# Optimization experiments

Measured on AMD Instinct MI355X. Metric: run time of the kernel, lower is better.

Reference implementation:

```python
import math
import jax, jax.numpy as jnp
import numpy as np

B, L, D_MODEL, H = 8, 4096, 1024, 16
D_HEAD = D_MODEL // H
FACTOR = 5
U = max(int(math.ceil(math.log(L))) * FACTOR, 1)  # 45 = sample_k = n_top


def setup_inputs() -> dict:
    key = jax.random.key(0)
    ks = jax.random.split(key, 12)
    s = 0.02
    return {
        "Q": jax.random.normal(ks[0], (B, L, D_MODEL), jnp.float32),
        "K": jax.random.normal(ks[1], (B, L, D_MODEL), jnp.float32),
        "V": jax.random.normal(ks[2], (B, L, D_MODEL), jnp.float32),
        "Wq": jax.random.normal(ks[3], (D_MODEL, D_MODEL), jnp.float32) * s,
        "bq": jnp.zeros((D_MODEL,), jnp.float32),
        "Wk": jax.random.normal(ks[4], (D_MODEL, D_MODEL), jnp.float32) * s,
        "bk": jnp.zeros((D_MODEL,), jnp.float32),
        "Wv": jax.random.normal(ks[5], (D_MODEL, D_MODEL), jnp.float32) * s,
        "bv": jnp.zeros((D_MODEL,), jnp.float32),
        "Wo": jax.random.normal(ks[6], (D_MODEL, D_MODEL), jnp.float32) * s,
        "bo": jnp.zeros((D_MODEL,), jnp.float32),
        "index_sample": jax.random.randint(ks[7], (U,), 0, L, dtype=jnp.int32),
    }


def reference(Q, K, V, Wq, bq, Wk, bk, Wv, bv, Wo, bo, index_sample):
    scale = 1.0 / math.sqrt(D_HEAD)
    # projections (torch Linear: x @ W.T + b), split into heads -> [B,H,L,D]
    q = (Q @ Wq.T + bq).reshape(B, L, H, D_HEAD).transpose(0, 2, 1, 3)
    k = (K @ Wk.T + bk).reshape(B, L, H, D_HEAD).transpose(0, 2, 1, 3)
    v = (V @ Wv.T + bv).reshape(B, L, H, D_HEAD).transpose(0, 2, 1, 3)
    # _prob_QK: sample U keys, score every query against them
    k_samp = k[:, :, index_sample, :]                        # [B,H,U,D]
    qk_samp = jnp.einsum('bhqd,bhsd->bhqs', q, k_samp)       # [B,H,L,U]
    M = qk_samp.max(-1) - qk_samp.mean(-1)                   # [B,H,L] max-mean sparsity metric
    _, m_top = jax.lax.top_k(M, U)                           # [B,H,U] top query indices
    # gather top queries, reduced attention over ALL keys
    q_red = jnp.take_along_axis(q, m_top[..., None], axis=2)  # [B,H,U,D]
    scores = jnp.einsum('bhud,bhkd->bhuk', q_red, k) * scale  # [B,H,U,L]
    attn = jax.nn.softmax(scores, axis=-1)
    ctx = jnp.einsum('bhuk,bhkd->bhud', attn, v)              # [B,H,U,D]
    ctx_mean = ctx.mean(axis=2)                               # [B,H,D]
    ctx_flat = ctx_mean.transpose(0, 2, 1).reshape(B, D_MODEL)  # transpose(1,2).view(B,-1)
    return ctx_flat @ Wo.T + bo                               # [B, d_model]
```

## Files before the change

kernel.cpp:

```cpp
#include <hip/hip_runtime.h>
#include <stdint.h>

#define B_ 8
#define L_ 4096
#define DM_ 1024
#define H_ 16
#define DH_ 64
#define U_ 45
#define BH_ 128
#define GROWS_ 384
#define GM_ 3072
#define CHUNKS_ 2

typedef unsigned short u16;
typedef unsigned int u32;
typedef __attribute__((ext_vector_type(8))) short short8;
typedef __attribute__((ext_vector_type(4))) float f32x4;
typedef __attribute__((ext_vector_type(8))) float f32x8;

__device__ __forceinline__ u16 f2bf_rne(float x){
  u32 u = __float_as_uint(x);
  return (u16)((u + 0x7FFFu + ((u >> 16) & 1u)) >> 16);
}
__device__ __forceinline__ float bf2f(u16 v){ return __uint_as_float(((u32)v) << 16); }

__device__ __forceinline__ void gload_lds16(const void* g, void* l){
  auto gp = (const __attribute__((address_space(1))) u32*)(uintptr_t)g;
  auto lp = (__attribute__((address_space(3))) u32*)(u32)(uintptr_t)l;
  __builtin_amdgcn_global_load_lds(gp, lp, 16, 0, 0);
}

__device__ __forceinline__ void split1(float x, u16& h, u16& l){
  h = f2bf_rne(x);
  l = f2bf_rne(x - bf2f(h));
}

__global__ void prep_w(const float* __restrict__ Wq, const float* __restrict__ Wk,
                       const float* __restrict__ Wv,
                       u16* __restrict__ WQH, u16* __restrict__ WQL,
                       u16* __restrict__ WKH, u16* __restrict__ WKL,
                       u16* __restrict__ WVH){
  const int i = (blockIdx.x * 256 + threadIdx.x) * 4;
  float4 a; ushort4 h, l;
  a = *(const float4*)(Wq + i);
  split1(a.x, h.x, l.x); split1(a.y, h.y, l.y); split1(a.z, h.z, l.z); split1(a.w, h.w, l.w);
  *(ushort4*)(WQH + i) = h; *(ushort4*)(WQL + i) = l;
  a = *(const float4*)(Wk + i);
  split1(a.x, h.x, l.x); split1(a.y, h.y, l.y); split1(a.z, h.z, l.z); split1(a.w, h.w, l.w);
  *(ushort4*)(WKH + i) = h; *(ushort4*)(WKL + i) = l;
  a = *(const float4*)(Wv + i);
  split1(a.x, h.x, l.x); split1(a.y, h.y, l.y); split1(a.z, h.z, l.z); split1(a.w, h.w, l.w);
  *(ushort4*)(WVH + i) = h;
}

__global__ void gather_rows(const float* __restrict__ K, const int* __restrict__ IDX,
                            float* __restrict__ GATH){
  const int blk = blockIdx.x;
  const int b = blk / U_, u = blk % U_;
  const int t = threadIdx.x;
  const int row = IDX[u];
  const float4* src = (const float4*)(K + ((size_t)b * L_ + row) * DM_);
  float4* dst = (float4*)(GATH + ((size_t)(b * GROWS_ + u)) * DM_);
  dst[t] = src[t];
}

template<int PASSES, int OUTMODE>
__launch_bounds__(256, 2)
__global__ void gemm_proj(const float* __restrict__ A, const u16* __restrict__ BHp,
                          const u16* __restrict__ BLp, const float* __restrict__ bias,
                          void* __restrict__ outp){
  const int n0 = blockIdx.x * 128;
  const int m0 = blockIdx.y * 128;
  const int t = threadIdx.x;
  const int w = t >> 6, lane = t & 63;
  const int wr = w >> 1, wc = w & 1;

  __shared__ __attribute__((aligned(16))) float As[128 * 64];
  __shared__ __attribute__((aligned(16))) u16   Bhs[128 * 64];
  __shared__ __attribute__((aligned(16))) u16   Bls[(PASSES == 3) ? (128 * 64) : 64];

  f32x4 acc[4][4];
#pragma unroll
  for (int i = 0; i < 4; i++)
#pragma unroll
    for (int j = 0; j < 4; j++) acc[i][j] = (f32x4){0.f, 0.f, 0.f, 0.f};

  const int arow = lane >> 4;
  const int acol = (lane & 15) * 4;
  const int brow = lane >> 3;
  const int bcol = (lane & 7) * 8;

  for (int kt = 0; kt < 16; kt++){
    const int k0 = kt * 64;
#pragma unroll
    for (int ii = 0; ii < 8; ii++){
      const int nn = w * 8 + ii;
      const float* gp = A + (size_t)(m0 + 4 * nn + arow) * DM_ + (k0 + acol);
      gload_lds16(gp, As + nn * 256);
    }
#pragma unroll
    for (int ii = 0; ii < 4; ii++){
      const int nn = w * 4 + ii;
      const size_t go = (size_t)(n0 + 8 * nn + brow) * DM_ + (k0 + bcol);
      gload_lds16(BHp + go, Bhs + nn * 512);
      if constexpr (PASSES == 3) gload_lds16(BLp + go, Bls + nn * 512);
    }
    __syncthreads();

#pragma unroll
    for (int ks = 0; ks < 2; ks++){
      const int kk = ks * 32 + (lane >> 4) * 8;
      short8 ah[4], al[4];
#pragma unroll
      for (int i = 0; i < 4; i++){
        const float* ap = As + (wr * 64 + i * 16 + (lane & 15)) * 64 + kk;
        f32x8 x = *(const f32x8*)ap;
        short8 h, l;
#pragma unroll
        for (int c = 0; c < 8; c++){
          const u32 ub = __float_as_uint(x[c]);
          h[c] = (short)(ub >> 16);
          if constexpr (PASSES == 3){
            const float r = x[c] - __uint_as_float(ub & 0xFFFF0000u);
            l[c] = (short)(__float_as_uint(r) >> 16);
          }
        }
        ah[i] = h;
        if constexpr (PASSES == 3) al[i] = l;
      }
      short8 bh8[4], bl8[4];
#pragma unroll
      for (int j = 0; j < 4; j++){
        const int bo = (wc * 64 + j * 16 + (lane & 15)) * 64 + kk;
        bh8[j] = *(const short8*)(Bhs + bo);
        if constexpr (PASSES == 3) bl8[j] = *(const short8*)(Bls + bo);
      }
#pragma unroll
      for (int i = 0; i < 4; i++)
#pragma unroll
        for (int j = 0; j < 4; j++){
          acc[i][j] = __builtin_amdgcn_mfma_f32_16x16x32_bf16(ah[i], bh8[j], acc[i][j], 0, 0, 0);
          if constexpr (PASSES == 3){
            acc[i][j] = __builtin_amdgcn_mfma_f32_16x16x32_bf16(ah[i], bl8[j], acc[i][j], 0, 0, 0);
            acc[i][j] = __builtin_amdgcn_mfma_f32_16x16x32_bf16(al[i], bh8[j], acc[i][j], 0, 0, 0);
          }
        }
    }
    __syncthreads();
  }

  if constexpr (OUTMODE == 3){
    u16* tb = (u16*)As;
    const int b = m0 >> 12;
    const int l0 = m0 & 4095;
#pragma unroll
    for (int p = 0; p < 2; p++){
      if (wc == p){
#pragma unroll
        for (int j = 0; j < 4; j++){
          const int cl = j * 16 + (lane & 15);
          const float bv = bias[n0 + p * 64 + cl];
#pragma unroll
          for (int i = 0; i < 4; i++){
#pragma unroll
            for (int r = 0; r < 4; r++){
              const int gl = wr * 64 + i * 16 + (lane >> 4) * 4 + r;
              tb[cl * 136 + gl] = f2bf_rne(acc[i][j][r] + bv);
            }
          }
        }
      }
      __syncthreads();
      {
        const int cl = t >> 2;
        const int c = n0 + p * 64 + cl;
        const int h = c >> 6, d = c & 63;
        u16* dst = (u16*)outp + ((size_t)((b * H_ + h) * DH_ + d)) * L_ + l0;
#pragma unroll
        for (int k = 0; k < 4; k++){
          const int ch = (t & 3) + k * 4;
          *(short8*)(dst + ch * 8) = *(const short8*)(tb + cl * 136 + ch * 8);
        }
      }
      __syncthreads();
    }
  } else {
#pragma unroll
    for (int j = 0; j < 4; j++){
      const int c = n0 + wc * 64 + j * 16 + (lane & 15);
      const float bv = bias[c];
#pragma unroll
      for (int i = 0; i < 4; i++){
        const int mb = m0 + wr * 64 + i * 16 + (lane >> 4) * 4;
#pragma unroll
        for (int r = 0; r < 4; r++){
          const int g = mb + r;
          const float val = acc[i][j][r] + bv;
          if constexpr (OUTMODE == 2){
            ((float*)outp)[(size_t)g * DM_ + c] = val;
          } else {
            const int b = g >> 12, l2 = g & 4095;
            const int h = c >> 6, d = c & 63;
            const size_t oi = (((size_t)(b * H_ + h)) * L_ + l2) * DH_ + d;
            if constexpr (OUTMODE == 0) ((float*)outp)[oi] = val;
            else ((u16*)outp)[oi] = (u16)(__float_as_uint(val) >> 16);
          }
        }
      }
    }
  }
}

__global__ void compute_m(const float* __restrict__ QF, const float* __restrict__ KSAMP,
                          float* __restrict__ MBUF){
  const int bx = blockIdx.x;
  const int bh = bx >> 4, lp = bx & 15;
  const int b = bh >> 4, h = bh & 15;
  const int t = threadIdx.x;
  __shared__ float ks[U_ * DH_];
  for (int i = t; i < U_ * DH_; i += 256){
    const int u = i >> 6, d = i & 63;
    ks[i] = KSAMP[((size_t)(b * GROWS_ + u)) * DM_ + h * DH_ + d];
  }
  __syncthreads();
  const int l = lp * 256 + t;
  const float* q = QF + ((size_t)bh * L_ + l) * DH_;
  float4 qv[16];
#pragma unroll
  for (int c = 0; c < 16; c++) qv[c] = *(const float4*)(q + c * 4);
  float mx = -1e30f, sm = 0.f;
  for (int u = 0; u < U_; u++){
    const float* kp = ks + u * 64;
    float acc = 0.f;
#pragma unroll
    for (int c = 0; c < 16; c++){
      const float4 kv = *(const float4*)(kp + c * 4);
      acc += qv[c].x * kv.x + qv[c].y * kv.y + qv[c].z * kv.z + qv[c].w * kv.w;
    }
    mx = fmaxf(mx, acc); sm += acc;
  }
  MBUF[(size_t)bh * L_ + l] = mx - sm * (1.0f / 45.0f);
}

__global__ void topk45(const float* __restrict__ MBUF, int* __restrict__ MTOP){
  const int bh = blockIdx.x;
  const int t = threadIdx.x;
  __shared__ float Mv[L_];
  __shared__ float rv[256];
  __shared__ int ri[256];
  for (int i = t; i < L_; i += 256) Mv[i] = MBUF[(size_t)bh * L_ + i];
  __syncthreads();
  for (int it = 0; it < U_; it++){
    float bv = -1e30f; int bi = 0;
#pragma unroll
    for (int c = 0; c < 16; c++){
      const int idx = t * 16 + c;
      const float v = Mv[idx];
      if (v > bv){ bv = v; bi = idx; }
    }
    rv[t] = bv; ri[t] = bi;
    __syncthreads();
    for (int off = 128; off > 0; off >>= 1){
      if (t < off){
        const float v2 = rv[t + off]; const int i2 = ri[t + off];
        if (v2 > rv[t] || (v2 == rv[t] && i2 < ri[t])){ rv[t] = v2; ri[t] = i2; }
      }
      __syncthreads();
    }
    if (t == 0){ MTOP[bh * U_ + it] = ri[0]; Mv[ri[0]] = -1e30f; }
    __syncthreads();
  }
}

__launch_bounds__(256, 2)
__global__ void attn_fused(const float* __restrict__ QF, const u16* __restrict__ KB,
                           const u16* __restrict__ VT, const int* __restrict__ MTOP,
                           float* __restrict__ MLP, float* __restrict__ CTXP){
  const int bh = blockIdx.x;
  const int chunk = blockIdx.y;
  const int t = threadIdx.x, w = t >> 6, lane = t & 63;
  const int m16 = lane & 15, q4 = lane >> 4;

  __shared__ __attribute__((aligned(16))) float qs[48 * 68];
  __shared__ __attribute__((aligned(16))) u16 ps[4][48 * 72];

  for (int i = t; i < 48 * 64; i += 256){
    const int r = i >> 6, d = i & 63;
    float v = 0.f;
    if (r < U_) v = QF[((size_t)bh * L_ + MTOP[bh * U_ + r]) * DH_ + d] * 0.125f;
    qs[r * 68 + d] = v;
  }
  __syncthreads();

  short8 qh[3][2], ql[3][2];
#pragma unroll
  for (int i = 0; i < 3; i++)
#pragma unroll
    for (int ks = 0; ks < 2; ks++){
      const float* ap = qs + (i * 16 + m16) * 68 + ks * 32 + q4 * 8;
      f32x8 x = *(const f32x8*)ap;
      short8 h, l;
#pragma unroll
      for (int c = 0; c < 8; c++){
        const u32 ub = __float_as_uint(x[c]);
        h[c] = (short)(ub >> 16);
        const float r = x[c] - __uint_as_float(ub & 0xFFFF0000u);
        l[c] = (short)(__float_as_uint(r) >> 16);
      }
      qh[i][ks] = h; ql[i][ks] = l;
    }

  float m_run[3][4], l_run[3][4];
  f32x4 O[3][4];
#pragma unroll
  for (int i = 0; i < 3; i++)
#pragma unroll
    for (int r = 0; r < 4; r++){
      m_run[i][r] = -1e30f; l_run[i][r] = 0.f;
      O[i][r] = (f32x4){0.f, 0.f, 0.f, 0.f};
    }

  const u16* kb = KB + (size_t)bh * L_ * DH_;
  const u16* vt = VT + (size_t)bh * DH_ * L_;
  const int TPW = L_ / (CHUNKS_ * 4 * 64);
  u16* pw = ps[w];

  for (int tt = 0; tt < TPW; tt++){
    const int t0 = ((chunk * 4 + w) * TPW + tt) * 64;
    f32x4 S[3][4];
#pragma unroll
    for (int i = 0; i < 3; i++)
#pragma unroll
      for (int jt = 0; jt < 4; jt++) S[i][jt] = (f32x4){0.f, 0.f, 0.f, 0.f};
#pragma unroll
    for (int ks = 0; ks < 2; ks++){
      short8 kf[4];
#pragma unroll
      for (int jt = 0; jt < 4; jt++)
        kf[jt] = *(const short8*)(kb + (size_t)(t0 + jt * 16 + m16) * DH_ + ks * 32 + q4 * 8);
#pragma unroll
      for (int i = 0; i < 3; i++)
#pragma unroll
        for (int jt = 0; jt < 4; jt++){
          S[i][jt] = __builtin_amdgcn_mfma_f32_16x16x32_bf16(qh[i][ks], kf[jt], S[i][jt], 0, 0, 0);
          S[i][jt] = __builtin_amdgcn_mfma_f32_16x16x32_bf16(ql[i][ks], kf[jt], S[i][jt], 0, 0, 0);
        }
    }
#pragma unroll
    for (int i = 0; i < 3; i++){
      float mnew[4], alpha[4], psum[4];
#pragma unroll
      for (int r = 0; r < 4; r++){
        float mx = fmaxf(fmaxf(S[i][0][r], S[i][1][r]), fmaxf(S[i][2][r], S[i][3][r]));
        mx = fmaxf(mx, __shfl_xor(mx, 1));
        mx = fmaxf(mx, __shfl_xor(mx, 2));
        mx = fmaxf(mx, __shfl_xor(mx, 4));
        mx = fmaxf(mx, __shfl_xor(mx, 8));
        mnew[r] = fmaxf(m_run[i][r], mx);
        alpha[r] = __expf(m_run[i][r] - mnew[r]);
        m_run[i][r] = mnew[r];
        l_run[i][r] *= alpha[r];
        psum[r] = 0.f;
      }
#pragma unroll
      for (int jo = 0; jo < 4; jo++)
#pragma unroll
        for (int r = 0; r < 4; r++) O[i][jo][r] *= alpha[r];
#pragma unroll
      for (int jt = 0; jt < 4; jt++)
#pragma unroll
        for (int r = 0; r < 4; r++){
          const float pv = __expf(S[i][jt][r] - mnew[r]);
          const u16 pq = f2bf_rne(pv);
          psum[r] += bf2f(pq);
          pw[(i * 16 + q4 * 4 + r) * 72 + jt * 16 + m16] = pq;
        }
#pragma unroll
      for (int r = 0; r < 4; r++){
        float s = psum[r];
        s += __shfl_xor(s, 1); s += __shfl_xor(s, 2);
        s += __shfl_xor(s, 4); s += __shfl_xor(s, 8);
        l_run[i][r] += s;
      }
    }
#pragma unroll
    for (int ks = 0; ks < 2; ks++){
      short8 pa[3], vf[4];
#pragma unroll
      for (int i = 0; i < 3; i++)
        pa[i] = *(const short8*)(pw + (i * 16 + m16) * 72 + ks * 32 + q4 * 8);
#pragma unroll
      for (int jo = 0; jo < 4; jo++)
        vf[jo] = *(const short8*)(vt + (size_t)(jo * 16 + m16) * L_ + t0 + ks * 32 + q4 * 8);
#pragma unroll
      for (int i = 0; i < 3; i++)
#pragma unroll
        for (int jo = 0; jo < 4; jo++)
          O[i][jo] = __builtin_amdgcn_mfma_f32_16x16x32_bf16(pa[i], vf[jo], O[i][jo], 0, 0, 0);
    }
  }

  const int state = (bh * CHUNKS_ + chunk) * 4 + w;
  float* mlp = MLP + (size_t)state * 48 * 2;
  float* ctxp = CTXP + (size_t)state * 48 * 64;
#pragma unroll
  for (int i = 0; i < 3; i++)
#pragma unroll
    for (int r = 0; r < 4; r++){
      const int row = i * 16 + q4 * 4 + r;
      if (m16 == 0){ mlp[row * 2] = m_run[i][r]; mlp[row * 2 + 1] = l_run[i][r]; }
#pragma unroll
      for (int jo = 0; jo < 4; jo++)
        ctxp[row * 64 + jo * 16 + m16] = O[i][jo][r];
    }
}

__global__ void attn_combine(const float* __restrict__ MLP, const float* __restrict__ CTXP,
                             float* __restrict__ CTXF){
  const int bh = blockIdx.x;
  const int b = bh >> 4, h = bh & 15;
  const int t = threadIdx.x;
  const int col = t & 63, rg = t >> 6;
  const int NS = CHUNKS_ * 4;
  __shared__ float ml[8 * 48 * 2];
  __shared__ float red[4][64];
  for (int i = t; i < NS * 48 * 2; i += 256) ml[i] = MLP[(size_t)bh * NS * 48 * 2 + i];
  __syncthreads();
  float acc = 0.f;
  for (int rr = 0; rr < 12; rr++){
    const int row = rg * 12 + rr;
    if (row >= U_) break;
    float M = -1e30f;
#pragma unroll
    for (int s = 0; s < NS; s++) M = fmaxf(M, ml[s * 96 + row * 2]);
    float num = 0.f, den = 0.f;
#pragma unroll
    for (int s = 0; s < NS; s++){
      const float wgt = __expf(ml[s * 96 + row * 2] - M);
      num += wgt * CTXP[((size_t)bh * NS + s) * 48 * 64 + row * 64 + col];
      den += wgt * ml[s * 96 + row * 2 + 1];
    }
    acc += num / den;
  }
  red[rg][col] = acc;
  __syncthreads();
  if (t < 64){
    const float v = (red[0][t] + red[1][t] + red[2][t] + red[3][t]) * (1.0f / 45.0f);
    CTXF[b * DM_ + t * H_ + h] = v;
  }
}

__global__ void s4_out(const float* __restrict__ CTXF, const float* __restrict__ Wo,
                       const float* __restrict__ bo, float* __restrict__ out){
  const int jb = blockIdx.x;
  const int b = blockIdx.y;
  const int t = threadIdx.x;
  __shared__ float cx[DM_];
  for (int i = t; i < DM_; i += 256) cx[i] = CTXF[b * DM_ + i];
  __syncthreads();
  const int j = jb * 256 + t;
  const float* wrow = Wo + (size_t)j * DM_;
  float acc = bo[j];
  for (int c = 0; c < 256; c++){
    const float4 wv = *(const float4*)(wrow + c * 4);
    const float4 cv = *(const float4*)(cx + c * 4);
    acc += wv.x * cv.x + wv.y * cv.y + wv.z * cv.z + wv.w * cv.w;
  }
  out[b * DM_ + j] = acc;
}

extern "C" void kernel_launch(void* const* d_in, const int* in_sizes, int n_in,
                              void* d_out, int out_size, void* d_ws, size_t ws_size,
                              hipStream_t stream){
  const float* Q  = (const float*)d_in[0];
  const float* K  = (const float*)d_in[1];
  const float* V  = (const float*)d_in[2];
  const float* Wq = (const float*)d_in[3];
  const float* bq = (const float*)d_in[4];
  const float* Wk = (const float*)d_in[5];
  const float* bk = (const float*)d_in[6];
  const float* Wv = (const float*)d_in[7];
  const float* bv = (const float*)d_in[8];
  const float* Wo = (const float*)d_in[9];
  const float* bo = (const float*)d_in[10];
  const int* IDX  = (const int*)d_in[11];
  float* out = (float*)d_out;

  char* p = (char*)d_ws;
  auto alloc = [&](size_t bytes) -> char* {
    char* r = p; p += (bytes + 255) & ~(size_t)255; return r;
  };
  u16*  WQH  = (u16*)alloc((size_t)DM_ * DM_ * 2);
  u16*  WQL  = (u16*)alloc((size_t)DM_ * DM_ * 2);
  u16*  WKH  = (u16*)alloc((size_t)DM_ * DM_ * 2);
  u16*  WKL  = (u16*)alloc((size_t)DM_ * DM_ * 2);
  u16*  WVH  = (u16*)alloc((size_t)DM_ * DM_ * 2);
  float* QF  = (float*)alloc((size_t)BH_ * L_ * DH_ * 4);
  u16*  KB   = (u16*)alloc((size_t)BH_ * L_ * DH_ * 2);
  u16*  VT   = (u16*)alloc((size_t)BH_ * DH_ * L_ * 2);
  float* GATH = (float*)alloc((size_t)GM_ * DM_ * 4);
  float* KSAMP= (float*)alloc((size_t)GM_ * DM_ * 4);
  float* MBUF = (float*)alloc((size_t)BH_ * L_ * 4);
  int*   MTOP = (int*)alloc((size_t)BH_ * U_ * 4);
  float* MLP  = (float*)alloc((size_t)BH_ * CHUNKS_ * 4 * 48 * 2 * 4);
  float* CTXP = (float*)alloc((size_t)BH_ * CHUNKS_ * 4 * 48 * 64 * 4);
  float* CTXF = (float*)alloc((size_t)B_ * DM_ * 4);

  prep_w<<<dim3(1024), dim3(256), 0, stream>>>(Wq, Wk, Wv, WQH, WQL, WKH, WKL, WVH);
  gather_rows<<<dim3(B_ * U_), dim3(256), 0, stream>>>(K, IDX, GATH);
  gemm_proj<3, 0><<<dim3(8, 256), dim3(256), 0, stream>>>(Q, WQH, WQL, bq, (void*)QF);
  gemm_proj<1, 1><<<dim3(8, 256), dim3(256), 0, stream>>>(K, WKH, (const u16*)nullptr, bk, (void*)KB);
  gemm_proj<1, 3><<<dim3(8, 256), dim3(256), 0, stream>>>(V, WVH, (const u16*)nullptr, bv, (void*)VT);
  gemm_proj<3, 2><<<dim3(8, GM_ / 128), dim3(256), 0, stream>>>(GATH, WKH, WKL, bk, (void*)KSAMP);
  compute_m<<<dim3(BH_ * 16), dim3(256), 0, stream>>>(QF, KSAMP, MBUF);
  topk45<<<dim3(BH_), dim3(256), 0, stream>>>(MBUF, MTOP);
  attn_fused<<<dim3(BH_, CHUNKS_), dim3(256), 0, stream>>>(QF, KB, VT, MTOP, MLP, CTXP);
  attn_combine<<<dim3(BH_), dim3(256), 0, stream>>>(MLP, CTXP, CTXF);
  s4_out<<<dim3(4, 8), dim3(256), 0, stream>>>(CTXF, Wo, bo, out);
}
```

Baseline: 1.187 ms.

## Fuse max-mean sparsity metric into Q projection epilogue and swizzle GEMM LDS

The sampled-key score computation (compute_m) moves into the Q projection GEMM epilogue. Each block stages its projected Q tile in LDS and scores it against pre-split bf16 hi/lo sampled keys with MFMA, writing the max-mean metric directly. This drops the separate kernel and its re-read of QF. The sampled-key GEMM now runs on a padded 48-row gather (3 row blocks instead of 24), and a new ksprep kernel splits it into hi/lo bf16. GEMM LDS tiles get XOR swizzling to avoid bank conflicts, and topk uses wave shuffles instead of an LDS tree reduction. The cost is a larger LDS footprint for the Q GEMM (68KB), which could lower occupancy.

```diff
diff --git a/kernel.cpp b/kernel.cpp
--- a/kernel.cpp
+++ b/kernel.cpp
@@ -8,15 +8,12 @@
 #define DH_ 64
 #define U_ 45
 #define BH_ 128
-#define GROWS_ 384
-#define GM_ 3072
 #define CHUNKS_ 2
 
 typedef unsigned short u16;
 typedef unsigned int u32;
 typedef __attribute__((ext_vector_type(8))) short short8;
 typedef __attribute__((ext_vector_type(4))) float f32x4;
-typedef __attribute__((ext_vector_type(8))) float f32x8;
 
 __device__ __forceinline__ u16 f2bf_rne(float x){
   u32 u = __float_as_uint(x);
@@ -56,28 +53,35 @@
 __global__ void gather_rows(const float* __restrict__ K, const int* __restrict__ IDX,
                             float* __restrict__ GATH){
   const int blk = blockIdx.x;
-  const int b = blk / U_, u = blk % U_;
+  const int b = blk / 48, u = blk % 48;
   const int t = threadIdx.x;
-  const int row = IDX[u];
-  const float4* src = (const float4*)(K + ((size_t)b * L_ + row) * DM_);
-  float4* dst = (float4*)(GATH + ((size_t)(b * GROWS_ + u)) * DM_);
-  dst[t] = src[t];
-}
-
-template<int PASSES, int OUTMODE>
+  float4 v = make_float4(0.f, 0.f, 0.f, 0.f);
+  if (u < U_){
+    const int row = IDX[u];
+    v = ((const float4*)(K + ((size_t)b * L_ + row) * DM_))[t];
+  }
+  ((float4*)(GATH + ((size_t)(b * 48 + u)) * DM_))[t] = v;
+}
+
+template<int PASSES, int OUTMODE, bool WITHM>
 __launch_bounds__(256, 2)
 __global__ void gemm_proj(const float* __restrict__ A, const u16* __restrict__ BHp,
                           const u16* __restrict__ BLp, const float* __restrict__ bias,
-                          void* __restrict__ outp){
+                          void* __restrict__ outp,
+                          const u16* __restrict__ KSH, const u16* __restrict__ KSL,
+                          float* __restrict__ MBUF){
+  constexpr int LDSB = WITHM ? 69632 : (PASSES == 3 ? 65536 : 49152);
+  __shared__ __attribute__((aligned(16))) char smem[LDSB];
+  float* As = (float*)smem;
+  u16* Bhs = (u16*)(smem + 32768);
+  u16* Bls = (u16*)(smem + 49152);
+
   const int n0 = blockIdx.x * 128;
   const int m0 = blockIdx.y * 128;
   const int t = threadIdx.x;
   const int w = t >> 6, lane = t & 63;
   const int wr = w >> 1, wc = w & 1;
-
-  __shared__ __attribute__((aligned(16))) float As[128 * 64];
-  __shared__ __attribute__((aligned(16))) u16   Bhs[128 * 64];
-  __shared__ __attribute__((aligned(16))) u16   Bls[(PASSES == 3) ? (128 * 64) : 64];
+  const int m16 = lane & 15, q4 = lane >> 4;
 
   f32x4 acc[4][4];
 #pragma unroll
@@ -86,22 +90,26 @@
     for (int j = 0; j < 4; j++) acc[i][j] = (f32x4){0.f, 0.f, 0.f, 0.f};
 
   const int arow = lane >> 4;
-  const int acol = (lane & 15) * 4;
+  const int acN  = lane & 15;
   const int brow = lane >> 3;
-  const int bcol = (lane & 7) * 8;
+  const int bcN  = lane & 7;
 
   for (int kt = 0; kt < 16; kt++){
     const int k0 = kt * 64;
 #pragma unroll
     for (int ii = 0; ii < 8; ii++){
       const int nn = w * 8 + ii;
-      const float* gp = A + (size_t)(m0 + 4 * nn + arow) * DM_ + (k0 + acol);
+      const int rl = 4 * nn + arow;
+      const int c2 = acN ^ (rl & 15);
+      const float* gp = A + (size_t)(m0 + rl) * DM_ + (k0 + c2 * 4);
       gload_lds16(gp, As + nn * 256);
     }
 #pragma unroll
     for (int ii = 0; ii < 4; ii++){
       const int nn = w * 4 + ii;
-      const size_t go = (size_t)(n0 + 8 * nn + brow) * DM_ + (k0 + bcol);
+      const int rb = 8 * nn + brow;
+      const int cb = bcN ^ (brow & 7);
+      const size_t go = (size_t)(n0 + rb) * DM_ + (k0 + cb * 8);
       gload_lds16(BHp + go, Bhs + nn * 512);
       if constexpr (PASSES == 3) gload_lds16(BLp + go, Bls + nn * 512);
     }
@@ -109,31 +117,35 @@
 
 #pragma unroll
     for (int ks = 0; ks < 2; ks++){
-      const int kk = ks * 32 + (lane >> 4) * 8;
+      const int gc0 = ks * 8 + q4 * 2;
       short8 ah[4], al[4];
 #pragma unroll
       for (int i = 0; i < 4; i++){
-        const float* ap = As + (wr * 64 + i * 16 + (lane & 15)) * 64 + kk;
-        f32x8 x = *(const f32x8*)ap;
+        const float* base = As + (wr * 64 + i * 16 + m16) * 64;
+        const f32x4 xlo = *(const f32x4*)(base + (gc0 ^ m16) * 4);
+        const f32x4 xhi = *(const f32x4*)(base + ((gc0 + 1) ^ m16) * 4);
+        float xx[8] = {xlo[0], xlo[1], xlo[2], xlo[3], xhi[0], xhi[1], xhi[2], xhi[3]};
         short8 h, l;
 #pragma unroll
         for (int c = 0; c < 8; c++){
-          const u32 ub = __float_as_uint(x[c]);
+          const u32 ub = __float_as_uint(xx[c]);
           h[c] = (short)(ub >> 16);
           if constexpr (PASSES == 3){
-            const float r = x[c] - __uint_as_float(ub & 0xFFFF0000u);
+            const float r = xx[c] - __uint_as_float(ub & 0xFFFF0000u);
             l[c] = (short)(__float_as_uint(r) >> 16);
           }
         }
         ah[i] = h;
         if constexpr (PASSES == 3) al[i] = l;
       }
+      const int gcb = ks * 4 + q4;
       short8 bh8[4], bl8[4];
 #pragma unroll
       for (int j = 0; j < 4; j++){
-        const int bo = (wc * 64 + j * 16 + (lane & 15)) * 64 + kk;
-        bh8[j] = *(const short8*)(Bhs + bo);
-        if constexpr (PASSES == 3) bl8[j] = *(const short8*)(Bls + bo);
+        const int rowb = wc * 64 + j * 16 + m16;
+        const int pos = gcb ^ (m16 & 7);
+        bh8[j] = *(const short8*)(Bhs + rowb * 64 + pos * 8);
+        if constexpr (PASSES == 3) bl8[j] = *(const short8*)(Bls + rowb * 64 + pos * 8);
       }
 #pragma unroll
       for (int i = 0; i < 4; i++)
@@ -149,8 +161,9 @@
     __syncthreads();
   }
 
+  float* mt = (float*)smem + w * (64 * 68);
   if constexpr (OUTMODE == 3){
-    u16* tb = (u16*)As;
+    u16* tb = (u16*)smem;
     const int b = m0 >> 12;
     const int l0 = m0 & 4095;
 #pragma unroll
@@ -158,13 +171,13 @@
       if (wc == p){
 #pragma unroll
         for (int j = 0; j < 4; j++){
-          const int cl = j * 16 + (lane & 15);
+          const int cl = j * 16 + m16;
           const float bv = bias[n0 + p * 64 + cl];
 #pragma unroll
           for (int i = 0; i < 4; i++){
 #pragma unroll
             for (int r = 0; r < 4; r++){
-              const int gl = wr * 64 + i * 16 + (lane >> 4) * 4 + r;
+              const int gl = wr * 64 + i * 16 + q4 * 4 + r;
               tb[cl * 136 + gl] = f2bf_rne(acc[i][j][r] + bv);
             }
           }
@@ -187,11 +200,11 @@
   } else {
 #pragma unroll
     for (int j = 0; j < 4; j++){
-      const int c = n0 + wc * 64 + j * 16 + (lane & 15);
+      const int c = n0 + wc * 64 + j * 16 + m16;
       const float bv = bias[c];
 #pragma unroll
       for (int i = 0; i < 4; i++){
-        const int mb = m0 + wr * 64 + i * 16 + (lane >> 4) * 4;
+        const int mb = m0 + wr * 64 + i * 16 + q4 * 4;
 #pragma unroll
         for (int r = 0; r < 4; r++){
           const int g = mb + r;
@@ -205,69 +218,123 @@
             if constexpr (OUTMODE == 0) ((float*)outp)[oi] = val;
             else ((u16*)outp)[oi] = (u16)(__float_as_uint(val) >> 16);
           }
-        }
-      }
-    }
-  }
-}
-
-__global__ void compute_m(const float* __restrict__ QF, const float* __restrict__ KSAMP,
-                          float* __restrict__ MBUF){
-  const int bx = blockIdx.x;
-  const int bh = bx >> 4, lp = bx & 15;
+          if constexpr (WITHM)
+            mt[(i * 16 + q4 * 4 + r) * 68 + (j * 16 + m16)] = val;
+        }
+      }
+    }
+  }
+
+  if constexpr (WITHM){
+    const int bb = m0 >> 12;
+    const int head = (n0 >> 6) + wc;
+    const int bh2 = bb * H_ + head;
+    f32x4 S[4][3];
+#pragma unroll
+    for (int im = 0; im < 4; im++)
+#pragma unroll
+      for (int jt = 0; jt < 3; jt++) S[im][jt] = (f32x4){0.f, 0.f, 0.f, 0.f};
+#pragma unroll
+    for (int ks = 0; ks < 2; ks++){
+      short8 kh3[3], kl3[3];
+#pragma unroll
+      for (int jt = 0; jt < 3; jt++){
+        const size_t ko = ((size_t)bh2 * 48 + jt * 16 + m16) * 64 + ks * 32 + q4 * 8;
+        kh3[jt] = *(const short8*)(KSH + ko);
+        kl3[jt] = *(const short8*)(KSL + ko);
+      }
+#pragma unroll
+      for (int im = 0; im < 4; im++){
+        const float* ap = mt + (im * 16 + m16) * 68 + ks * 32 + q4 * 8;
+        const f32x4 xlo = *(const f32x4*)ap;
+        const f32x4 xhi = *(const f32x4*)(ap + 4);
+        float xx[8] = {xlo[0], xlo[1], xlo[2], xlo[3], xhi[0], xhi[1], xhi[2], xhi[3]};
+        short8 qh, ql;
+#pragma unroll
+        for (int c = 0; c < 8; c++){
+          const u32 ub = __float_as_uint(xx[c]);
+          qh[c] = (short)(ub >> 16);
+          const float r = xx[c] - __uint_as_float(ub & 0xFFFF0000u);
+          ql[c] = (short)(__float_as_uint(r) >> 16);
+        }
+#pragma unroll
+        for (int jt = 0; jt < 3; jt++){
+          S[im][jt] = __builtin_amdgcn_mfma_f32_16x16x32_bf16(qh, kh3[jt], S[im][jt], 0, 0, 0);
+          S[im][jt] = __builtin_amdgcn_mfma_f32_16x16x32_bf16(qh, kl3[jt], S[im][jt], 0, 0, 0);
+          S[im][jt] = __builtin_amdgcn_mfma_f32_16x16x32_bf16(ql, kh3[jt], S[im][jt], 0, 0, 0);
+        }
+      }
+    }
+#pragma unroll
+    for (int im = 0; im < 4; im++)
+#pragma unroll
+      for (int r = 0; r < 4; r++){
+        float mx = -1e30f, sm = 0.f;
+#pragma unroll
+        for (int jt = 0; jt < 3; jt++){
+          const bool ok = (jt < 2) || (m16 < 13);
+          const float v = S[im][jt][r];
+          if (ok){ mx = fmaxf(mx, v); sm += v; }
+        }
+#pragma unroll
+        for (int off = 1; off < 16; off <<= 1){
+          mx = fmaxf(mx, __shfl_xor(mx, off));
+          sm += __shfl_xor(sm, off);
+        }
+        if (m16 == 0){
+          const int l2 = (m0 & 4095) + wr * 64 + im * 16 + q4 * 4 + r;
+          MBUF[(size_t)bh2 * L_ + l2] = mx - sm * (1.0f / 45.0f);
+        }
+      }
+  }
+}
+
+__global__ void ksprep(const float* __restrict__ KSAMP, u16* __restrict__ KSH,
+                       u16* __restrict__ KSL){
+  const int bh = blockIdx.x;
   const int b = bh >> 4, h = bh & 15;
   const int t = threadIdx.x;
-  __shared__ float ks[U_ * DH_];
-  for (int i = t; i < U_ * DH_; i += 256){
+  for (int i = t; i < 48 * 64; i += 256){
     const int u = i >> 6, d = i & 63;
-    ks[i] = KSAMP[((size_t)(b * GROWS_ + u)) * DM_ + h * DH_ + d];
-  }
-  __syncthreads();
-  const int l = lp * 256 + t;
-  const float* q = QF + ((size_t)bh * L_ + l) * DH_;
-  float4 qv[16];
-#pragma unroll
-  for (int c = 0; c < 16; c++) qv[c] = *(const float4*)(q + c * 4);
-  float mx = -1e30f, sm = 0.f;
-  for (int u = 0; u < U_; u++){
-    const float* kp = ks + u * 64;
-    float acc = 0.f;
-#pragma unroll
-    for (int c = 0; c < 16; c++){
-      const float4 kv = *(const float4*)(kp + c * 4);
-      acc += qv[c].x * kv.x + qv[c].y * kv.y + qv[c].z * kv.z + qv[c].w * kv.w;
-    }
-    mx = fmaxf(mx, acc); sm += acc;
-  }
-  MBUF[(size_t)bh * L_ + l] = mx - sm * (1.0f / 45.0f);
+    const float v = (u < U_) ? KSAMP[(size_t)(b * 48 + u) * DM_ + h * DH_ + d] : 0.f;
+    u16 hh, ll; split1(v, hh, ll);
+    KSH[(size_t)bh * 48 * 64 + i] = hh;
+    KSL[(size_t)bh * 48 * 64 + i] = ll;
+  }
 }
 
 __global__ void topk45(const float* __restrict__ MBUF, int* __restrict__ MTOP){
   const int bh = blockIdx.x;
-  const int t = threadIdx.x;
+  const int t = threadIdx.x, w = t >> 6, lane = t & 63;
   __shared__ float Mv[L_];
-  __shared__ float rv[256];
-  __shared__ int ri[256];
+  __shared__ float rv[4];
+  __shared__ int ri[4];
   for (int i = t; i < L_; i += 256) Mv[i] = MBUF[(size_t)bh * L_ + i];
   __syncthreads();
   for (int it = 0; it < U_; it++){
     float bv = -1e30f; int bi = 0;
 #pragma unroll
     for (int c = 0; c < 16; c++){
-      const int idx = t * 16 + c;
+      const int idx = c * 256 + t;
       const float v = Mv[idx];
-      if (v > bv){ bv = v; bi = idx; }
-    }
-    rv[t] = bv; ri[t] = bi;
+      if (v > bv || (v == bv && idx < bi)){ bv = v; bi = idx; }
+    }
+#pragma unroll
+    for (int off = 1; off < 64; off <<= 1){
+      const float ov = __shfl_xor(bv, off);
+      const int oi = __shfl_xor(bi, off);
+      if (ov > bv || (ov == bv && oi < bi)){ bv = ov; bi = oi; }
+    }
+    if (lane == 0){ rv[w] = bv; ri[w] = bi; }
     __syncthreads();
-    for (int off = 128; off > 0; off >>= 1){
-      if (t < off){
-        const float v2 = rv[t + off]; const int i2 = ri[t + off];
-        if (v2 > rv[t] || (v2 == rv[t] && i2 < ri[t])){ rv[t] = v2; ri[t] = i2; }
-      }
-      __syncthreads();
-    }
-    if (t == 0){ MTOP[bh * U_ + it] = ri[0]; Mv[ri[0]] = -1e30f; }
+    if (t == 0){
+      float fb = rv[0]; int fi = ri[0];
+#pragma unroll
+      for (int s = 1; s < 4; s++)
+        if (rv[s] > fb || (rv[s] == fb && ri[s] < fi)){ fb = rv[s]; fi = ri[s]; }
+      MTOP[bh * U_ + it] = fi;
+      Mv[fi] = -1e30f;
+    }
     __syncthreads();
   }
 }
@@ -298,13 +365,15 @@
 #pragma unroll
     for (int ks = 0; ks < 2; ks++){
       const float* ap = qs + (i * 16 + m16) * 68 + ks * 32 + q4 * 8;
-      f32x8 x = *(const f32x8*)ap;
+      const f32x4 xlo = *(const f32x4*)ap;
+      const f32x4 xhi = *(const f32x4*)(ap + 4);
+      float xx[8] = {xlo[0], xlo[1], xlo[2], xlo[3], xhi[0], xhi[1], xhi[2], xhi[3]};
       short8 h, l;
 #pragma unroll
       for (int c = 0; c < 8; c++){
-        const u32 ub = __float_as_uint(x[c]);
+        const u32 ub = __float_as_uint(xx[c]);
         h[c] = (short)(ub >> 16);
-        const float r = x[c] - __uint_as_float(ub & 0xFFFF0000u);
+        const float r = xx[c] - __uint_as_float(ub & 0xFFFF0000u);
         l[c] = (short)(__float_as_uint(r) >> 16);
       }
       qh[i][ks] = h; ql[i][ks] = l;
@@ -498,8 +567,10 @@
   float* QF  = (float*)alloc((size_t)BH_ * L_ * DH_ * 4);
   u16*  KB   = (u16*)alloc((size_t)BH_ * L_ * DH_ * 2);
   u16*  VT   = (u16*)alloc((size_t)BH_ * DH_ * L_ * 2);
-  float* GATH = (float*)alloc((size_t)GM_ * DM_ * 4);
-  float* KSAMP= (float*)alloc((size_t)GM_ * DM_ * 4);
+  float* GATH = (float*)alloc((size_t)B_ * 48 * DM_ * 4);
+  float* KSAMP= (float*)alloc((size_t)B_ * 48 * DM_ * 4);
+  u16*  KSH  = (u16*)alloc((size_t)BH_ * 48 * DH_ * 2);
+  u16*  KSL  = (u16*)alloc((size_t)BH_ * 48 * DH_ * 2);
   float* MBUF = (float*)alloc((size_t)BH_ * L_ * 4);
   int*   MTOP = (int*)alloc((size_t)BH_ * U_ * 4);
   float* MLP  = (float*)alloc((size_t)BH_ * CHUNKS_ * 4 * 48 * 2 * 4);
@@ -507,12 +578,16 @@
   float* CTXF = (float*)alloc((size_t)B_ * DM_ * 4);
 
   prep_w<<<dim3(1024), dim3(256), 0, stream>>>(Wq, Wk, Wv, WQH, WQL, WKH, WKL, WVH);
-  gather_rows<<<dim3(B_ * U_), dim3(256), 0, stream>>>(K, IDX, GATH);
-  gemm_proj<3, 0><<<dim3(8, 256), dim3(256), 0, stream>>>(Q, WQH, WQL, bq, (void*)QF);
-  gemm_proj<1, 1><<<dim3(8, 256), dim3(256), 0, stream>>>(K, WKH, (const u16*)nullptr, bk, (void*)KB);
-  gemm_proj<1, 3><<<dim3(8, 256), dim3(256), 0, stream>>>(V, WVH, (const u16*)nullptr, bv, (void*)VT);
-  gemm_proj<3, 2><<<dim3(8, GM_ / 128), dim3(256), 0, stream>>>(GATH, WKH, WKL, bk, (void*)KSAMP);
-  compute_m<<<dim3(BH_ * 16), dim3(256), 0, stream>>>(QF, KSAMP, MBUF);
+  gather_rows<<<dim3(B_ * 48), dim3(256), 0, stream>>>(K, IDX, GATH);
+  gemm_proj<3, 2, false><<<dim3(8, 3), dim3(256), 0, stream>>>(
+      GATH, WKH, WKL, bk, (void*)KSAMP, nullptr, nullptr, nullptr);
+  ksprep<<<dim3(BH_), dim3(256), 0, stream>>>(KSAMP, KSH, KSL);
+  gemm_proj<3, 0, true><<<dim3(8, 256), dim3(256), 0, stream>>>(
+      Q, WQH, WQL, bq, (void*)QF, KSH, KSL, MBUF);
+  gemm_proj<1, 1, false><<<dim3(8, 256), dim3(256), 0, stream>>>(
+      K, WKH, nullptr, bk, (void*)KB, nullptr, nullptr, nullptr);
+  gemm_proj<1, 3, false><<<dim3(8, 256), dim3(256), 0, stream>>>(
+      V, WVH, nullptr, bv, (void*)VT, nullptr, nullptr, nullptr);
   topk45<<<dim3(BH_), dim3(256), 0, stream>>>(MBUF, MTOP);
   attn_fused<<<dim3(BH_, CHUNKS_), dim3(256), 0, stream>>>(QF, KB, VT, MTOP, MLP, CTXP);
   attn_combine<<<dim3(BH_), dim3(256), 0, stream>>>(MLP, CTXP, CTXF);
```

Measured after the change: 997.5 us. 16.0% less time.
